# Kernel tuning notes

Measured on AMD Instinct MI355X. Metric: run time of the kernel, lower is better.

Reference implementation:

```python
import jax, jax.numpy as jnp
import numpy as np

B, S, D, H = 4, 2048, 1024, 16
HD = D // H  # 64


def setup_inputs() -> dict:
    key = jax.random.key(0)
    ks = jax.random.split(key, 11)
    scale = 1.0 / np.sqrt(D)
    inp = {
        "query": jax.random.normal(ks[0], (B, S, D), jnp.float32),
        "key": jax.random.normal(ks[1], (B, S, D), jnp.float32),
        "value": jax.random.normal(ks[2], (B, S, D), jnp.float32),
        "mask": jnp.ones((B, 1, 1, S), jnp.float32),
        "wq": jax.random.normal(ks[3], (D, D), jnp.float32) * scale,
        "bq": jnp.zeros((D,), jnp.float32),
        "wk": jax.random.normal(ks[4], (D, D), jnp.float32) * scale,
        "bk": jnp.zeros((D,), jnp.float32),
        "wv": jax.random.normal(ks[5], (D, D), jnp.float32) * scale,
        "bv": jnp.zeros((D,), jnp.float32),
        "wo": jax.random.normal(ks[6], (D, D), jnp.float32) * scale,
        "bo": jnp.zeros((D,), jnp.float32),
    }
    return inp


def reference(query, key, value, mask, wq, bq, wk, bk, wv, bv, wo, bo):
    b = query.shape[0]
    # Dense QKV projections
    q = query @ wq + bq  # [B,S,D]
    k = key @ wk + bk
    v = value @ wv + bv

    def split_heads(x):
        return x.reshape(b, -1, H, HD).transpose(0, 2, 1, 3)  # [B,H,S,HD]

    q, k, v = split_heads(q), split_heads(k), split_heads(v)
    score = jnp.einsum("bhqd,bhkd->bhqk", q, k) / jnp.sqrt(jnp.float32(HD))
    score = score + (1.0 - mask) * -1e9
    alpha = jax.nn.softmax(score, axis=-1)
    context = jnp.einsum("bhqk,bhkd->bhqd", alpha, v)  # [B,H,S,HD]
    context = context.transpose(0, 2, 1, 3).reshape(b, -1, D)
    return context @ wo + bo
```

## Files before the change

### kernel.cpp

```cpp
#include <hip/hip_runtime.h>

using u16 = unsigned short;
using u32 = unsigned int;

typedef float  f32x4  __attribute__((ext_vector_type(4)));
typedef float  f32x16 __attribute__((ext_vector_type(16)));
typedef u32    u32x4  __attribute__((ext_vector_type(4)));
typedef _Float16 f16;
typedef f16 f16x8 __attribute__((ext_vector_type(8)));

#define DEVI static __device__ __forceinline__

constexpr int S_  = 2048;
constexpr int D_  = 1024;
constexpr int HD_ = 64;
constexpr int SH_ = S_*HD_;
constexpr size_t NE_ = 8192ull*1024ull;

DEVI f32x4 mfma16f(f16x8 a, f16x8 b, f32x4 c){
  return __builtin_amdgcn_mfma_f32_16x16x32_f16(a, b, c, 0, 0, 0);
}
DEVI f32x16 mfma32(f16x8 a, f16x8 b, f32x16 c){
  return __builtin_amdgcn_mfma_f32_32x32x16_f16(a, b, c, 0, 0, 0);
}
DEVI float exp2fast(float x){
#if __has_builtin(__builtin_amdgcn_exp2f)
  return __builtin_amdgcn_exp2f(x);
#else
  float r; asm("v_exp_f32 %0, %1" : "=v"(r) : "v"(x)); return r;
#endif
}
DEVI float rcpfast(float x){
#if __has_builtin(__builtin_amdgcn_rcpf)
  return __builtin_amdgcn_rcpf(x);
#else
  float r; asm("v_rcp_f32 %0, %1" : "=v"(r) : "v"(x)); return r;
#endif
}
DEVI u32 pkh(float a, float b){
  return __builtin_bit_cast(u32, __builtin_amdgcn_cvt_pkrtz(a, b));
}
DEVI void gld16(const void* g, void* l){
  __builtin_amdgcn_global_load_lds(
      (const __attribute__((address_space(1))) u32*)g,
      (__attribute__((address_space(3))) u32*)l, 16, 0, 0);
}
DEVI void gld4(const void* g, void* l){
  __builtin_amdgcn_global_load_lds(
      (const __attribute__((address_space(1))) u32*)g,
      (__attribute__((address_space(3))) u32*)l, 4, 0, 0);
}

__global__ __launch_bounds__(256) void wcvt_k(
    const float* __restrict__ wq, const float* __restrict__ wk,
    const float* __restrict__ wv, const float* __restrict__ wo,
    u16* __restrict__ wt)
{
  int z = blockIdx.z;
  const float* W = (z==0)?wq:(z==1)?wk:(z==2)?wv:wo;
  u16* ot = wt + (size_t)z*D_*D_;
  __shared__ float t[64][65];
  int k0 = blockIdx.y*64, n0 = blockIdx.x*64;
  int tid = threadIdx.x;
#pragma unroll
  for (int i=0;i<4;i++){
    int lin = i*256 + tid;
    int r = lin>>4, c = (lin&15)*4;
    f32x4 v = *reinterpret_cast<const f32x4*>(W + (size_t)(k0+r)*D_ + n0 + c);
    t[r][c+0]=v.x; t[r][c+1]=v.y; t[r][c+2]=v.z; t[r][c+3]=v.w;
  }
  __syncthreads();
  int n = tid>>2, c0 = (tid&3)*16;
  alignas(16) u16 hb[16];
#pragma unroll
  for (int i=0;i<16;i++) hb[i] = __builtin_bit_cast(u16, (f16)t[c0+i][n]);
  size_t off = (size_t)(n0+n)*D_ + k0 + c0;
  *reinterpret_cast<u32x4*>(ot+off)   = *reinterpret_cast<u32x4*>(hb);
  *reinterpret_cast<u32x4*>(ot+off+8) = *reinterpret_cast<u32x4*>(hb+8);
}

__global__ __launch_bounds__(256) void acvt_k(
    const float* __restrict__ q, const float* __restrict__ k,
    const float* __restrict__ v, u16* __restrict__ out)
{
  int z = blockIdx.y;
  const float* src = (z==0)?q:(z==1)?k:v;
  u16* dst = out + (size_t)z*NE_;
  size_t i = ((size_t)blockIdx.x*256 + threadIdx.x)*8;
  f32x4 a = *reinterpret_cast<const f32x4*>(src + i);
  f32x4 b = *reinterpret_cast<const f32x4*>(src + i + 4);
  u32x4 t;
  t.x = pkh(a.x,a.y); t.y = pkh(a.z,a.w);
  t.z = pkh(b.x,b.y); t.w = pkh(b.z,b.w);
  *reinterpret_cast<u32x4*>(dst + i) = t;
}

__global__ __launch_bounds__(256) void madd_k(const float* __restrict__ mask,
                                              float* __restrict__ madd2)
{
  int i = blockIdx.x*256 + threadIdx.x;
  if (i < 4*S_) madd2[i] = (1.0f - mask[i]) * -1442695040.0f;
}

struct GemmArgs {
  const void* A[3];
  const u16*  Wt[3];
  const float* bias[3];
  float*      outF[3];
  u16*        outH[3];
  float       scale[3];
  int         mode[3];
};

__global__ __launch_bounds__(512, 4) void gemm_k(GemmArgs args)
{
  int z = blockIdx.z;
  const u16*   __restrict__ A    = (const u16*)args.A[z];
  const u16*   __restrict__ Wt   = args.Wt[z];
  const float* __restrict__ bias = args.bias[z];
  int mode = args.mode[z];
  float sc = args.scale[z];

  constexpr int ABYT = 16384;
  constexpr int BUFS = ABYT + 8192;
  __shared__ __align__(16) unsigned char smem[73728];
  char* sbase = (char*)smem;

  int m0 = blockIdx.x*256, n0 = blockIdx.y*128;
  int tid = threadIdx.x, lane = tid&63, w = tid>>6;
  int wm = (w>>1)*64, wn = (w&1)*64;
  int lr = lane&15, lh = lane>>4;

  int offA[2], offB;
#pragma unroll
  for (int j=0;j<2;j++){
    int chunk = w*2 + j;
    int row = chunk*16 + (lane>>2);
    int gs = lane&3;
    offA[j] = row*D_ + (((gs - (row>>1)) & 3)*8);
  }
  {
    int row = w*16 + (lane>>2);
    int gs = lane&3;
    offB = row*D_ + (((gs - (row>>1)) & 3)*8);
  }

  f32x4 acc[4][4];
#pragma unroll
  for (int m=0;m<4;m++)
#pragma unroll
    for (int n=0;n<4;n++) acc[m][n] = f32x4{0.f,0.f,0.f,0.f};

  auto STAGE = [&](int buf, int kt){
    char* lA = sbase + buf*BUFS;
    char* lB = lA + ABYT;
    const u16* As = A  + (size_t)m0*D_ + kt*32;
#pragma unroll
    for (int j=0;j<2;j++) gld16(As + offA[j], lA + (w*2+j)*1024);
    const u16* Bs = Wt + (size_t)n0*D_ + kt*32;
    gld16(Bs + offB, lB + w*1024);
  };

  STAGE(0, 0);
  STAGE(1, 1);
  STAGE(2, 2);

  for (int kt=0; kt<32; ++kt){
    int buf = kt - (kt/3)*3;
    if (kt < 30)       asm volatile("s_waitcnt vmcnt(6)" ::: "memory");
    else if (kt == 30) asm volatile("s_waitcnt vmcnt(3)" ::: "memory");
    else               asm volatile("s_waitcnt vmcnt(0)" ::: "memory");
    __builtin_amdgcn_s_barrier();

    char* bA = sbase + buf*BUFS;
    char* bB = bA + ABYT;
    f16x8 af[4], bfr[4];
#pragma unroll
    for (int m=0;m<4;m++){
      int row = wm + m*16 + lr;
      af[m] = *reinterpret_cast<const f16x8*>(bA + row*64 + (((lh + (row>>1)) & 3)<<4));
    }
#pragma unroll
    for (int n=0;n<4;n++){
      int row = wn + n*16 + lr;
      bfr[n] = *reinterpret_cast<const f16x8*>(bB + row*64 + (((lh + (row>>1)) & 3)<<4));
    }
    asm volatile("s_waitcnt lgkmcnt(0)" ::: "memory");
    __builtin_amdgcn_sched_barrier(0);
    __builtin_amdgcn_s_barrier();
    if (kt < 29) STAGE(buf, kt+3);

    __builtin_amdgcn_s_setprio(1);
#pragma unroll
    for (int m=0;m<4;m++)
#pragma unroll
      for (int n=0;n<4;n++)
        acc[m][n] = mfma16f(af[m], bfr[n], acc[m][n]);
    __builtin_amdgcn_s_setprio(0);
  }

  float bsetv[4];
#pragma unroll
  for (int n=0;n<4;n++) bsetv[n] = bias[n0 + wn + n*16 + lr];

  if (mode == 0){
    float* out = args.outF[z];
#pragma unroll
    for (int m=0;m<4;m++)
#pragma unroll
      for (int n=0;n<4;n++)
#pragma unroll
        for (int r=0;r<4;r++){
          int row = m0 + wm + m*16 + lh*4 + r;
          int col = n0 + wn + n*16 + lr;
          out[(size_t)row*D_ + col] = (acc[m][n][r] + bsetv[n])*sc;
        }
  } else if (mode == 1){
    u16* oh = args.outH[z];
#pragma unroll
    for (int m=0;m<4;m++)
#pragma unroll
      for (int n=0;n<4;n++)
#pragma unroll
        for (int r=0;r<4;r++){
          int row = m0 + wm + m*16 + lh*4 + r;
          int col = n0 + wn + n*16 + lr;
          float val = (acc[m][n][r] + bsetv[n])*sc;
          int b = row >> 11, s = row & 2047;
          int hh = col >> 6,  dd = col & 63;
          oh[(size_t)(b*16 + hh)*SH_ + (size_t)s*HD_ + dd] =
              __builtin_bit_cast(u16, (f16)val);
        }
  } else {
    __syncthreads();
    u16* ct = (u16*)sbase;
#pragma unroll
    for (int m=0;m<4;m++)
#pragma unroll
      for (int n=0;n<4;n++)
#pragma unroll
        for (int r=0;r<4;r++){
          int lrow = wm + m*16 + lh*4 + r;
          int lcol = wn + n*16 + lr;
          ct[lrow*132 + lcol] = __builtin_bit_cast(u16, (f16)((acc[m][n][r] + bsetv[n])*sc));
        }
    __syncthreads();
    u16* ovt = args.outH[z];
    int b = m0 >> 11, s0 = m0 & 2047;
    int ch = tid >> 2, quarter = tid & 3;
    int gn = n0 + ch;
    int hh = gn >> 6, dd = gn & 63;
    size_t obase = (size_t)(b*16 + hh)*SH_ + (size_t)dd*S_ + s0 + quarter*64;
#pragma unroll
    for (int i=0;i<8;i++){
      alignas(16) u16 tmp[8];
#pragma unroll
      for (int j=0;j<8;j++) tmp[j] = ct[(quarter*64 + i*8 + j)*132 + ch];
      *reinterpret_cast<u32x4*>(ovt + obase + i*8) = *reinterpret_cast<u32x4*>(tmp);
    }
  }
}

__global__ __launch_bounds__(256, 2) void attn_k(
    const f16* __restrict__ Qf, const f16* __restrict__ Kf,
    const f16* __restrict__ Vt, const float* __restrict__ madd2,
    u16* __restrict__ cf)
{
  constexpr int BUFS = 33280;
  __shared__ __align__(16) unsigned char smem[2*BUFS];
  char* sbase = (char*)smem;

  int flat = blockIdx.x + blockIdx.y*gridDim.x;
  int xcd = flat & 7, ix = flat >> 3;
  int bh = xcd + 8*(ix >> 4);
  int qx = ix & 15;
  int b = bh >> 4, head = bh & 15;

  const f16* Qb = Qf + (size_t)bh*SH_;
  const f16* Kb = Kf + (size_t)bh*SH_;
  const f16* Vb = Vt + (size_t)bh*SH_;
  const float* mb = madd2 + (size_t)b*S_;

  int tid = threadIdx.x, lane = tid&63, w = tid>>6;
  int q31 = lane&31, h = lane>>5;
  int qw = qx*128 + w*32;
  int xorv = (q31&7)<<4;

  f16x8 qb[4];
#pragma unroll
  for (int ks=0;ks<4;ks++)
    qb[ks] = *reinterpret_cast<const f16x8*>(Qb + (size_t)(qw + q31)*HD_ + ks*16 + h*8);

  int offK[4], offV[4];
#pragma unroll
  for (int j=0;j<4;j++){
    int L = (w*4+j)*1024 + lane*16;
    int rK = L>>7;
    int dbyK = (L&127) ^ ((rK&7)<<4);
    offK[j] = rK*HD_ + (dbyK>>1);
    int rV = L>>8;
    int dbyV = (L&255) ^ ((rV&7)<<4);
    offV[j] = rV*S_ + (dbyV>>1);
  }

  u32 one2 = 0x3C003C00u;
  u32x4 onev; onev.x=one2; onev.y=one2; onev.z=one2; onev.w=one2;
  f16x8 vones = __builtin_bit_cast(f16x8, onev);

  f32x16 z16;
#pragma unroll
  for (int r=0;r<16;r++) z16[r] = 0.f;

  f32x16 o[2], ol;
#pragma unroll
  for (int n=0;n<2;n++)
#pragma unroll
    for (int r=0;r<16;r++) o[n][r] = 0.f;
#pragma unroll
  for (int r=0;r<16;r++) ol[r] = 0.f;

  auto STAGE = [&](int buf, int t){
    int kv0 = t*128;
    char* sKb = sbase + buf*BUFS;
    char* sVb = sKb + 16384;
    char* sMb = sKb + 32768;
#pragma unroll
    for (int j=0;j<4;j++)
      gld16(Kb + (size_t)kv0*HD_ + offK[j], sKb + (w*4+j)*1024);
#pragma unroll
    for (int j=0;j<4;j++)
      gld16(Vb + kv0 + offV[j], sVb + (w*4+j)*1024);
    gld4(mb + kv0 + lane, sMb);
    gld4(mb + kv0 + 64 + lane, sMb + 256);
  };

  STAGE(0, 0);
  STAGE(1, 1);

  for (int t=0; t<16; ++t){
    int buf = t&1;
    char* sKb = sbase + buf*BUFS;
    char* sVb = sKb + 16384;
    float* sMb = (float*)(sKb + 32768);

    if (t < 15) asm volatile("s_waitcnt vmcnt(10)" ::: "memory");
    else        asm volatile("s_waitcnt vmcnt(0)"  ::: "memory");
    __builtin_amdgcn_s_barrier();
    __builtin_amdgcn_sched_barrier(0);

    f32x16 stA[2], stB[2];

    __builtin_amdgcn_s_setprio(1);
#pragma unroll
    for (int n=0;n<2;n++){
      int rb = (n*32 + q31)*128;
      f16x8 ka = *reinterpret_cast<const f16x8*>(sKb + ((rb + h*16) ^ xorv));
      stA[n] = mfma32(ka, qb[0], z16);
#pragma unroll
      for (int ks=1;ks<4;ks++){
        ka = *reinterpret_cast<const f16x8*>(sKb + ((rb + ks*32 + h*16) ^ xorv));
        stA[n] = mfma32(ka, qb[ks], stA[n]);
      }
    }
#pragma unroll
    for (int n=0;n<2;n++){
      int rb = (64 + n*32 + q31)*128;
      f16x8 ka = *reinterpret_cast<const f16x8*>(sKb + ((rb + h*16) ^ xorv));
      stB[n] = mfma32(ka, qb[0], z16);
#pragma unroll
      for (int ks=1;ks<4;ks++){
        ka = *reinterpret_cast<const f16x8*>(sKb + ((rb + ks*32 + h*16) ^ xorv));
        stB[n] = mfma32(ka, qb[ks], stB[n]);
      }
    }
    __builtin_amdgcn_s_setprio(0);

    auto SMPV = [&](int sub, f32x16 (&st)[2]){
      float mval = sMb[sub*64 + lane];
      if (__ballot(mval != 0.0f)){
#pragma unroll
        for (int n=0;n<2;n++)
#pragma unroll
          for (int g=0;g<4;g++){
            f32x4 mv = *reinterpret_cast<const f32x4*>(sMb + sub*64 + n*32 + g*8 + h*4);
#pragma unroll
            for (int c=0;c<4;c++) st[n][g*4+c] += mv[c];
          }
      }
#pragma unroll
      for (int n=0;n<2;n++)
#pragma unroll
        for (int r=0;r<16;r++) st[n][r] = exp2fast(st[n][r]);

      f16x8 pa[4];
#pragma unroll
      for (int n=0;n<2;n++){
        u32 x[4], y[4];
#pragma unroll
        for (int T=0;T<4;T++){
          x[T] = pkh(st[n][4*T+0], st[n][4*T+1]);
          y[T] = pkh(st[n][4*T+2], st[n][4*T+3]);
        }
#pragma unroll
        for (int k2=0;k2<2;k2++){
          u32 a0=x[2*k2], b0=x[2*k2+1], a1=y[2*k2], b1=y[2*k2+1];
          asm volatile("v_permlane32_swap_b32 %0, %1" : "+v"(a0), "+v"(b0));
          asm volatile("v_permlane32_swap_b32 %0, %1" : "+v"(a1), "+v"(b1));
          u32x4 wv;
          wv.x = a0;
          wv.y = a1;
          wv.z = b0;
          wv.w = b1;
          pa[2*n+k2] = __builtin_bit_cast(f16x8, wv);
        }
      }

      __builtin_amdgcn_s_setprio(1);
#pragma unroll
      for (int n=0;n<2;n++){
        int rbv = (n*32 + q31)*256 + sub*128;
#pragma unroll
        for (int ks=0;ks<4;ks++){
          f16x8 vbf = *reinterpret_cast<const f16x8*>(sVb + ((rbv + ks*32 + h*16) ^ xorv));
          o[n] = mfma32(pa[ks], vbf, o[n]);
        }
      }
#pragma unroll
      for (int ks=0;ks<4;ks++)
        ol = mfma32(pa[ks], vones, ol);
      __builtin_amdgcn_s_setprio(0);
    };

    SMPV(0, stA);
    SMPV(1, stB);

    asm volatile("s_waitcnt lgkmcnt(0)" ::: "memory");
    __builtin_amdgcn_s_barrier();
    __builtin_amdgcn_sched_barrier(0);
    if (t < 14) STAGE(buf, t+2);
  }

#pragma unroll
  for (int n=0;n<2;n++)
#pragma unroll
    for (int r=0;r<16;r++){
      float inv = rcpfast(ol[r]);
      int s = qw + (r&3) + 8*(r>>2) + 4*h;
      int d = head*HD_ + n*32 + q31;
      cf[((size_t)(b*S_ + s))*D_ + d] = __builtin_bit_cast(u16, (f16)(o[n][r]*inv));
    }
}

extern "C" void kernel_launch(void* const* d_in, const int* in_sizes, int n_in,
                              void* d_out, int out_size, void* d_ws, size_t ws_size,
                              hipStream_t stream)
{
  (void)in_sizes; (void)n_in; (void)out_size;
  const float* query=(const float*)d_in[0];
  const float* key  =(const float*)d_in[1];
  const float* value=(const float*)d_in[2];
  const float* mask =(const float*)d_in[3];
  const float* wq=(const float*)d_in[4];
  const float* bq=(const float*)d_in[5];
  const float* wk=(const float*)d_in[6];
  const float* bk=(const float*)d_in[7];
  const float* wv=(const float*)d_in[8];
  const float* bv=(const float*)d_in[9];
  const float* wo=(const float*)d_in[10];
  const float* bo=(const float*)d_in[11];
  float* out = (float*)d_out;

  const size_t WN = 4ull*1024*1024;
  size_t need = WN*2 + 3*NE_*2 + 3*NE_*2 + NE_*2 + 8192*4;
  if (ws_size < need) return;

  char* ws = (char*)d_ws;
  u16* wt = (u16*)ws;
  u16* aq = wt + WN;
  u16* ak = aq + NE_;
  u16* av = ak + NE_;
  u16* qf = av + NE_;
  u16* kf = qf + NE_;
  u16* vt = kf + NE_;
  u16* cf = vt + NE_;
  float* madd2 = (float*)(cf + NE_);

  const float CSC = 0.18033688011112042f;

  wcvt_k<<<dim3(16,16,4), 256, 0, stream>>>(wq,wk,wv,wo,wt);
  acvt_k<<<dim3(4096,3), 256, 0, stream>>>(query,key,value,aq);
  madd_k<<<dim3(32), 256, 0, stream>>>(mask, madd2);

  GemmArgs ga{};
  ga.A[0]=aq; ga.A[1]=ak; ga.A[2]=av;
  ga.Wt[0]=wt;           ga.Wt[1]=wt+1048576;   ga.Wt[2]=wt+2097152;
  ga.bias[0]=bq; ga.bias[1]=bk; ga.bias[2]=bv;
  ga.scale[0]=CSC; ga.scale[1]=1.0f; ga.scale[2]=1.0f;
  ga.mode[0]=1;  ga.mode[1]=1;  ga.mode[2]=2;
  ga.outH[0]=qf; ga.outH[1]=kf; ga.outH[2]=vt;
  gemm_k<<<dim3(32,8,3), 512, 0, stream>>>(ga);

  attn_k<<<dim3(16,64), 256, 0, stream>>>((const f16*)qf,(const f16*)kf,(const f16*)vt,madd2,cf);

  GemmArgs go{};
  go.A[0]=cf;
  go.Wt[0]=wt+3145728;
  go.bias[0]=bo; go.scale[0]=1.0f; go.mode[0]=0; go.outF[0]=out;
  gemm_k<<<dim3(32,8,1), 512, 0, stream>>>(go);
}
```

Before: 211.3 us.

## Fuse fp32-to-fp16 activation conversion into QKV projection GEMM loads

Removes the separate activation conversion kernel and has the QKV GEMM stage fp32 activations straight into shared memory, converting to fp16 when fragments are read. This removes a full write and re-read of the fp16 activation copies. In exchange the GEMM moves twice the A-tile bytes per stage, uses a larger LDS footprint, and drops from triple to double buffering, which may expose more load latency.

```diff
diff --git a/kernel.cpp b/kernel.cpp
--- a/kernel.cpp
+++ b/kernel.cpp
@@ -79,22 +79,6 @@
   *reinterpret_cast<u32x4*>(ot+off+8) = *reinterpret_cast<u32x4*>(hb+8);
 }
 
-__global__ __launch_bounds__(256) void acvt_k(
-    const float* __restrict__ q, const float* __restrict__ k,
-    const float* __restrict__ v, u16* __restrict__ out)
-{
-  int z = blockIdx.y;
-  const float* src = (z==0)?q:(z==1)?k:v;
-  u16* dst = out + (size_t)z*NE_;
-  size_t i = ((size_t)blockIdx.x*256 + threadIdx.x)*8;
-  f32x4 a = *reinterpret_cast<const f32x4*>(src + i);
-  f32x4 b = *reinterpret_cast<const f32x4*>(src + i + 4);
-  u32x4 t;
-  t.x = pkh(a.x,a.y); t.y = pkh(a.z,a.w);
-  t.z = pkh(b.x,b.y); t.w = pkh(b.z,b.w);
-  *reinterpret_cast<u32x4*>(dst + i) = t;
-}
-
 __global__ __launch_bounds__(256) void madd_k(const float* __restrict__ mask,
                                               float* __restrict__ madd2)
 {
@@ -112,18 +96,21 @@
   int         mode[3];
 };
 
+template<bool AF32>
 __global__ __launch_bounds__(512, 4) void gemm_k(GemmArgs args)
 {
   int z = blockIdx.z;
-  const u16*   __restrict__ A    = (const u16*)args.A[z];
+  const float* __restrict__ Af   = (const float*)args.A[z];
+  const u16*   __restrict__ Ah   = (const u16*)args.A[z];
   const u16*   __restrict__ Wt   = args.Wt[z];
   const float* __restrict__ bias = args.bias[z];
   int mode = args.mode[z];
   float sc = args.scale[z];
 
-  constexpr int ABYT = 16384;
+  constexpr int ABYT = AF32 ? 32768 : 16384;
   constexpr int BUFS = ABYT + 8192;
-  __shared__ __align__(16) unsigned char smem[73728];
+  constexpr int NBUF = AF32 ? 2 : 3;
+  __shared__ __align__(16) unsigned char smem[AF32 ? 81920 : 73728];
   char* sbase = (char*)smem;
 
   int m0 = blockIdx.x*256, n0 = blockIdx.y*128;
@@ -131,13 +118,23 @@
   int wm = (w>>1)*64, wn = (w&1)*64;
   int lr = lane&15, lh = lane>>4;
 
-  int offA[2], offB;
-#pragma unroll
-  for (int j=0;j<2;j++){
-    int chunk = w*2 + j;
-    int row = chunk*16 + (lane>>2);
-    int gs = lane&3;
-    offA[j] = row*D_ + (((gs - (row>>1)) & 3)*8);
+  int offA[4], offB;
+  if constexpr (AF32){
+#pragma unroll
+    for (int j=0;j<4;j++){
+      int chunk = w*4 + j;
+      int row = chunk*8 + (lane>>3);
+      int g = lane&7;
+      offA[j] = row*D_ + ((g ^ (row&7))*4);
+    }
+  } else {
+#pragma unroll
+    for (int j=0;j<2;j++){
+      int chunk = w*2 + j;
+      int row = chunk*16 + (lane>>2);
+      int gs = lane&3;
+      offA[j] = row*D_ + (((gs - (row>>1)) & 3)*8);
+    }
   }
   {
     int row = w*16 + (lane>>2);
@@ -154,22 +151,33 @@
   auto STAGE = [&](int buf, int kt){
     char* lA = sbase + buf*BUFS;
     char* lB = lA + ABYT;
-    const u16* As = A  + (size_t)m0*D_ + kt*32;
-#pragma unroll
-    for (int j=0;j<2;j++) gld16(As + offA[j], lA + (w*2+j)*1024);
+    if constexpr (AF32){
+      const float* As = Af + (size_t)m0*D_ + kt*32;
+#pragma unroll
+      for (int j=0;j<4;j++) gld16(As + offA[j], lA + (w*4+j)*1024);
+    } else {
+      const u16* As = Ah + (size_t)m0*D_ + kt*32;
+#pragma unroll
+      for (int j=0;j<2;j++) gld16(As + offA[j], lA + (w*2+j)*1024);
+    }
     const u16* Bs = Wt + (size_t)n0*D_ + kt*32;
     gld16(Bs + offB, lB + w*1024);
   };
 
   STAGE(0, 0);
   STAGE(1, 1);
-  STAGE(2, 2);
+  if constexpr (!AF32) STAGE(2, 2);
 
   for (int kt=0; kt<32; ++kt){
-    int buf = kt - (kt/3)*3;
-    if (kt < 30)       asm volatile("s_waitcnt vmcnt(6)" ::: "memory");
-    else if (kt == 30) asm volatile("s_waitcnt vmcnt(3)" ::: "memory");
-    else               asm volatile("s_waitcnt vmcnt(0)" ::: "memory");
+    int buf = kt - (kt/NBUF)*NBUF;
+    if constexpr (AF32){
+      if (kt < 31) asm volatile("s_waitcnt vmcnt(5)" ::: "memory");
+      else         asm volatile("s_waitcnt vmcnt(0)" ::: "memory");
+    } else {
+      if (kt < 30)       asm volatile("s_waitcnt vmcnt(6)" ::: "memory");
+      else if (kt == 30) asm volatile("s_waitcnt vmcnt(3)" ::: "memory");
+      else               asm volatile("s_waitcnt vmcnt(0)" ::: "memory");
+    }
     __builtin_amdgcn_s_barrier();
 
     char* bA = sbase + buf*BUFS;
@@ -178,7 +186,16 @@
 #pragma unroll
     for (int m=0;m<4;m++){
       int row = wm + m*16 + lr;
-      af[m] = *reinterpret_cast<const f16x8*>(bA + row*64 + (((lh + (row>>1)) & 3)<<4));
+      if constexpr (AF32){
+        f32x4 a0 = *reinterpret_cast<const f32x4*>(bA + row*128 + ((((lh<<1)  ) ^ (row&7))<<4));
+        f32x4 a1 = *reinterpret_cast<const f32x4*>(bA + row*128 + ((((lh<<1)|1) ^ (row&7))<<4));
+        u32x4 uw;
+        uw.x = pkh(a0.x,a0.y); uw.y = pkh(a0.z,a0.w);
+        uw.z = pkh(a1.x,a1.y); uw.w = pkh(a1.z,a1.w);
+        af[m] = __builtin_bit_cast(f16x8, uw);
+      } else {
+        af[m] = *reinterpret_cast<const f16x8*>(bA + row*64 + (((lh + (row>>1)) & 3)<<4));
+      }
     }
 #pragma unroll
     for (int n=0;n<4;n++){
@@ -188,7 +205,11 @@
     asm volatile("s_waitcnt lgkmcnt(0)" ::: "memory");
     __builtin_amdgcn_sched_barrier(0);
     __builtin_amdgcn_s_barrier();
-    if (kt < 29) STAGE(buf, kt+3);
+    if constexpr (AF32){
+      if (kt < 30) STAGE(buf, kt+2);
+    } else {
+      if (kt < 29) STAGE(buf, kt+3);
+    }
 
     __builtin_amdgcn_s_setprio(1);
 #pragma unroll
@@ -471,15 +492,12 @@
   float* out = (float*)d_out;
 
   const size_t WN = 4ull*1024*1024;
-  size_t need = WN*2 + 3*NE_*2 + 3*NE_*2 + NE_*2 + 8192*4;
+  size_t need = WN*2 + 4*NE_*2 + 8192*4;
   if (ws_size < need) return;
 
   char* ws = (char*)d_ws;
   u16* wt = (u16*)ws;
-  u16* aq = wt + WN;
-  u16* ak = aq + NE_;
-  u16* av = ak + NE_;
-  u16* qf = av + NE_;
+  u16* qf = wt + WN;
   u16* kf = qf + NE_;
   u16* vt = kf + NE_;
   u16* cf = vt + NE_;
@@ -488,17 +506,16 @@
   const float CSC = 0.18033688011112042f;
 
   wcvt_k<<<dim3(16,16,4), 256, 0, stream>>>(wq,wk,wv,wo,wt);
-  acvt_k<<<dim3(4096,3), 256, 0, stream>>>(query,key,value,aq);
   madd_k<<<dim3(32), 256, 0, stream>>>(mask, madd2);
 
   GemmArgs ga{};
-  ga.A[0]=aq; ga.A[1]=ak; ga.A[2]=av;
+  ga.A[0]=query; ga.A[1]=key; ga.A[2]=value;
   ga.Wt[0]=wt;           ga.Wt[1]=wt+1048576;   ga.Wt[2]=wt+2097152;
   ga.bias[0]=bq; ga.bias[1]=bk; ga.bias[2]=bv;
   ga.scale[0]=CSC; ga.scale[1]=1.0f; ga.scale[2]=1.0f;
   ga.mode[0]=1;  ga.mode[1]=1;  ga.mode[2]=2;
   ga.outH[0]=qf; ga.outH[1]=kf; ga.outH[2]=vt;
-  gemm_k<<<dim3(32,8,3), 512, 0, stream>>>(ga);
+  gemm_k<true><<<dim3(32,8,3), 512, 0, stream>>>(ga);
 
   attn_k<<<dim3(16,64), 256, 0, stream>>>((const f16*)qf,(const f16*)kf,(const f16*)vt,madd2,cf);
 
@@ -506,5 +523,5 @@
   go.A[0]=cf;
   go.Wt[0]=wt+3145728;
   go.bias[0]=bo; go.scale[0]=1.0f; go.mode[0]=0; go.outF[0]=out;
-  gemm_k<<<dim3(32,8,1), 512, 0, stream>>>(go);
-}
+  gemm_k<false><<<dim3(32,8,1), 512, 0, stream>>>(go);
+}
```

Measured after the change: 199.1 us. 1.06x faster.
